# Kernel tuning notes

Measured on AMD Instinct MI355X. Metric: run time of the kernel, lower is better.

## Reference

```python
import jax, jax.numpy as jnp
import numpy as np
from jax import lax

B_SZ, SEQ, D_MODEL = 8, 2048, 1024
N_LAYER = 2
D_INNER = 2 * D_MODEL          # expand=2
D_STATE = 16
D_CONV = 4
DT_RANK = D_MODEL // 16        # ceil(1024/16)=64
EPS = 1e-5


def setup_inputs() -> dict:
    key = jax.random.key(0)
    ks = jax.random.split(key, 8)
    f = lambda k, shp, sc: jax.random.normal(k, shp, jnp.float32) * sc
    A_log = jnp.tile(jnp.log(jnp.arange(1, D_STATE + 1, dtype=jnp.float32)),
                     (N_LAYER, D_INNER, 1))  # S4D-real init, [L, d_inner, d_state]
    return {
        "x": f(ks[0], (B_SZ, SEQ, D_MODEL), 1.0),
        "in_proj_w": f(ks[1], (N_LAYER, 2 * D_INNER, D_MODEL), 0.02),
        "conv_w": f(ks[2], (N_LAYER, D_INNER, D_CONV), 0.2),
        "conv_b": jnp.zeros((N_LAYER, D_INNER), jnp.float32),
        "x_proj_w": f(ks[3], (N_LAYER, DT_RANK + 2 * D_STATE, D_INNER), 0.02),
        "dt_proj_w": f(ks[4], (N_LAYER, D_INNER, DT_RANK), 0.1),
        "dt_proj_b": f(ks[5], (N_LAYER, D_INNER), 0.5) - 4.0,  # softplus -> small dt
        "A_log": A_log,
        "D_param": jnp.ones((N_LAYER, D_INNER), jnp.float32),
        "out_proj_w": f(ks[6], (N_LAYER, D_MODEL, D_INNER), 0.02),
        "norm_w": jnp.ones((N_LAYER, D_MODEL), jnp.float32),
        "norm_b": jnp.zeros((N_LAYER, D_MODEL), jnp.float32),
    }


def _layer_norm(x, w, b):
    mu = jnp.mean(x, axis=-1, keepdims=True)
    var = jnp.mean(jnp.square(x - mu), axis=-1, keepdims=True)
    return (x - mu) * lax.rsqrt(var + EPS) * w + b


def _causal_dw_conv(x, w, b):
    # x: [B, Lq, d_inner], w: [d_inner, d_conv] depthwise causal conv
    xp = jnp.pad(x, ((0, 0), (D_CONV - 1, 0), (0, 0)))
    L = x.shape[1]
    y = b
    for k in range(D_CONV):
        y = y + xp[:, k:k + L, :] * w[:, k]
    return y


def _selective_scan(u, dt, Bm, Cm, A, Dp):
    # u, dt: [B, Lq, d_inner]; Bm, Cm: [B, Lq, d_state]; A: [d_inner, d_state]
    def step(h, inp):
        ut, dtt, Bt, Ct = inp                         # [B,di],[B,di],[B,ds],[B,ds]
        dA = jnp.exp(dtt[..., None] * A)              # [B, di, ds]
        h = dA * h + (dtt * ut)[..., None] * Bt[:, None, :]
        y = jnp.einsum('bds,bs->bd', h, Ct)
        return h, y

    h0 = jnp.zeros((u.shape[0], D_INNER, D_STATE), u.dtype)
    xs = (u.transpose(1, 0, 2), dt.transpose(1, 0, 2),
          Bm.transpose(1, 0, 2), Cm.transpose(1, 0, 2))
    _, ys = lax.scan(step, h0, xs)                    # ys: [Lq, B, di]
    return ys.transpose(1, 0, 2) + u * Dp


def _mamba(x, in_w, cw, cb, xpw, dtw, dtb, A_log, Dp, ow):
    xz = jnp.einsum('bld,ed->ble', x, in_w)           # [B, L, 2*d_inner]
    xi, z = jnp.split(xz, 2, axis=-1)
    xc = jax.nn.silu(_causal_dw_conv(xi, cw, cb))     # [B, L, d_inner]
    xdbl = jnp.einsum('bld,ed->ble', xc, xpw)         # [B, L, dt_rank+2*d_state]
    dt_low = xdbl[..., :DT_RANK]
    Bm = xdbl[..., DT_RANK:DT_RANK + D_STATE]
    Cm = xdbl[..., DT_RANK + D_STATE:]
    dt = jax.nn.softplus(jnp.einsum('blr,dr->bld', dt_low, dtw) + dtb)
    A = -jnp.exp(A_log)                               # [d_inner, d_state]
    y = _selective_scan(xc, dt, Bm, Cm, A, Dp)
    y = y * jax.nn.silu(z)
    return jnp.einsum('ble,de->bld', y, ow)           # [B, L, d_model]


def reference(x, in_proj_w, conv_w, conv_b, x_proj_w, dt_proj_w, dt_proj_b,
              A_log, D_param, out_proj_w, norm_w, norm_b):
    residual = None
    for l in range(N_LAYER):
        residual = x if residual is None else x + residual
        h = _layer_norm(residual, norm_w[l], norm_b[l])
        x = _mamba(h, in_proj_w[l], conv_w[l], conv_b[l], x_proj_w[l],
                   dt_proj_w[l], dt_proj_b[l], A_log[l], D_param[l], out_proj_w[l])
    # NOTE: source forward returns x without applying norm_f
    return x
```

## Files before the change

### kernel.cpp

```cpp
#include <hip/hip_runtime.h>
#include <cstddef>
#include <cstdint>

#define SEQB   8
#define SEQL   2048
#define DMODEL 1024
#define DINNER 2048
#define DSTATE 16
#define NC     32
#define TC     64
#define TT     8

typedef __attribute__((ext_vector_type(4))) float f32x4;
typedef __attribute__((ext_vector_type(8))) short bf16x8;
typedef unsigned int u32;
typedef const __attribute__((address_space(1))) u32* gas_ptr;
typedef __attribute__((address_space(3))) u32* las_ptr;

__device__ __forceinline__ void gld16(const void* g, void* l){
  __builtin_amdgcn_global_load_lds((gas_ptr)g, (las_ptr)l, 16, 0, 0);
}

__device__ __forceinline__ float siluf(float x){ return x / (1.f + __expf(-x)); }
__device__ __forceinline__ float softplusf(float x){ return (x > 20.f) ? x : log1pf(__expf(x)); }

__device__ __forceinline__ unsigned short f2bf_rne(float f){
  unsigned int u = __float_as_uint(f);
  u += 0x7FFFu + ((u>>16)&1u);
  return (unsigned short)(u>>16);
}
__device__ __forceinline__ void split_bf(float f, unsigned short& h, unsigned short& l){
  unsigned short hs = f2bf_rne(f);
  float hf = __uint_as_float(((unsigned int)hs)<<16);
  h = hs;
  l = f2bf_rne(f - hf);
}

__global__ __launch_bounds__(256)
void wsplit2(const float* __restrict__ src, unsigned short* __restrict__ dst,
             int K, int k4shift)
{
  int idx = blockIdx.x*256 + threadIdx.x;
  int r  = idx >> k4shift;
  int c4 = idx & ((1<<k4shift)-1);
  float4 v = ((const float4*)src)[idx];
  unsigned short h,l; short4 h4, l4;
  split_bf(v.x,h,l); h4.x=(short)h; l4.x=(short)l;
  split_bf(v.y,h,l); h4.y=(short)h; l4.y=(short)l;
  split_bf(v.z,h,l); h4.z=(short)h; l4.z=(short)l;
  split_bf(v.w,h,l); h4.w=(short)h; l4.w=(short)l;
  size_t ro = (size_t)r*2*K;
  *(short4*)&dst[ro + (c4<<2)]     = h4;
  *(short4*)&dst[ro + K + (c4<<2)] = l4;
}

__global__ __launch_bounds__(256)
void wsplit_og(const float* __restrict__ src, unsigned short* __restrict__ dst)
{
  int idx = blockIdx.x*256 + threadIdx.x;
  int r  = idx >> 9;
  int c4 = idx & 511;
  int layer = r >> 10, rr = r & 1023;
  float4 v = ((const float4*)src)[idx];
  unsigned short h,l; short4 h4, l4;
  split_bf(v.x,h,l); h4.x=(short)h; l4.x=(short)l;
  split_bf(v.y,h,l); h4.y=(short)h; l4.y=(short)l;
  split_bf(v.z,h,l); h4.z=(short)h; l4.z=(short)l;
  split_bf(v.w,h,l); h4.w=(short)h; l4.w=(short)l;
  int col = c4 << 2;
  int g = col >> 8, j = col & 255;
  size_t base = (size_t)layer*1024*4096 + (size_t)rr*4096 + g*512 + j;
  *(short4*)&dst[base]       = h4;
  *(short4*)&dst[base + 256] = l4;
}

__global__ __launch_bounds__(256)
void ln_split2(const float* __restrict__ a, const float* __restrict__ res,
               const float* __restrict__ w, const float* __restrict__ bias,
               unsigned short* __restrict__ Hs)
{
  int row = blockIdx.x;
  size_t off = (size_t)row * DMODEL;
  float4 v = ((const float4*)(a + off))[threadIdx.x];
  if (res){
    float4 u = ((const float4*)(res + off))[threadIdx.x];
    v.x += u.x; v.y += u.y; v.z += u.z; v.w += u.w;
  }
  float s  = v.x + v.y + v.z + v.w;
  float s2 = fmaf(v.x,v.x, fmaf(v.y,v.y, fmaf(v.z,v.z, v.w*v.w)));
  #pragma unroll
  for (int o=32;o>0;o>>=1){ s += __shfl_down(s,o,64); s2 += __shfl_down(s2,o,64); }
  __shared__ float red[8];
  int lane = threadIdx.x & 63, wid = threadIdx.x >> 6;
  if (lane==0){ red[wid]=s; red[4+wid]=s2; }
  __syncthreads();
  s  = red[0]+red[1]+red[2]+red[3];
  s2 = red[4]+red[5]+red[6]+red[7];
  float mu  = s * (1.f/DMODEL);
  float var = s2 * (1.f/DMODEL) - mu*mu;
  float rstd = rsqrtf(var + 1e-5f);
  float4 wv = ((const float4*)w)[threadIdx.x];
  float4 bv = ((const float4*)bias)[threadIdx.x];
  float4 o4;
  o4.x = (v.x-mu)*rstd*wv.x + bv.x;
  o4.y = (v.y-mu)*rstd*wv.y + bv.y;
  o4.z = (v.z-mu)*rstd*wv.z + bv.z;
  o4.w = (v.w-mu)*rstd*wv.w + bv.w;
  unsigned short h,l; short4 h4, l4;
  split_bf(o4.x,h,l); h4.x=(short)h; l4.x=(short)l;
  split_bf(o4.y,h,l); h4.y=(short)h; l4.y=(short)l;
  split_bf(o4.z,h,l); h4.z=(short)h; l4.z=(short)l;
  split_bf(o4.w,h,l); h4.w=(short)h; l4.w=(short)l;
  size_t ro = (size_t)row*2048;
  int c = threadIdx.x<<2;
  *(short4*)&Hs[ro + c]        = h4;
  *(short4*)&Hs[ro + 1024 + c] = l4;
}

__global__ __launch_bounds__(256)
void mgemm_in(const unsigned short* __restrict__ A,
              const unsigned short* __restrict__ B,
              float* __restrict__ XI, float* __restrict__ ZB)
{
  __shared__ __align__(16) unsigned short As[128*64];
  __shared__ __align__(16) unsigned short Bs[128*64];
  const int t = threadIdx.x;
  const int mbase = blockIdx.y << 7, nbase = blockIdx.x << 7;

  const int lane = t & 63, w = t >> 6;
  const int wr = w >> 1, wc = w & 1;
  const int l16 = lane & 15, kq = lane >> 4;

  const int sr8 = lane >> 3, sl8 = lane & 7;
  const unsigned short* pA[4]; const unsigned short* pB[4];
  unsigned short* dA[4]; unsigned short* dB[4];
  #pragma unroll
  for (int c=0;c<4;c++){
    int row = c*32 + w*8 + sr8;
    int ss  = sl8 ^ (row & 7);
    int colb = (ss < 4) ? (ss<<3) : (1024 + ((ss-4)<<3));
    pA[c] = A + (size_t)(mbase+row)*2048 + colb;
    pB[c] = B + (size_t)(nbase+row)*2048 + colb;
    dA[c] = &As[row*64 + sl8*8];
    dB[c] = &Bs[row*64 + sl8*8];
  }

  f32x4 acc[4][4];
  #pragma unroll
  for (int i=0;i<4;i++)
    #pragma unroll
    for (int j=0;j<4;j++) acc[i][j] = (f32x4){0.f,0.f,0.f,0.f};

  for (int k0=0; k0<1024; k0+=32){
    #pragma unroll
    for (int c=0;c<4;c++){
      gld16(pA[c] + k0, dA[c]);
      gld16(pB[c] + k0, dB[c]);
    }
    __syncthreads();
    bf16x8 ah[4], al[4];
    #pragma unroll
    for (int mf=0; mf<4; mf++){
      int ra = wr*64 + mf*16 + l16;
      ah[mf] = *(const bf16x8*)&As[ra*64 + (( kq      ^ (ra&7))<<3)];
      al[mf] = *(const bf16x8*)&As[ra*64 + (((kq+4)   ^ (ra&7))<<3)];
    }
    #pragma unroll
    for (int nf=0; nf<4; nf++){
      int rb = wc*64 + nf*16 + l16;
      bf16x8 bh = *(const bf16x8*)&Bs[rb*64 + (( kq    ^ (rb&7))<<3)];
      bf16x8 bl = *(const bf16x8*)&Bs[rb*64 + (((kq+4) ^ (rb&7))<<3)];
      #pragma unroll
      for (int mf=0; mf<4; mf++){
        acc[mf][nf] = __builtin_amdgcn_mfma_f32_16x16x32_bf16(ah[mf], bh, acc[mf][nf], 0,0,0);
        acc[mf][nf] = __builtin_amdgcn_mfma_f32_16x16x32_bf16(ah[mf], bl, acc[mf][nf], 0,0,0);
        acc[mf][nf] = __builtin_amdgcn_mfma_f32_16x16x32_bf16(al[mf], bh, acc[mf][nf], 0,0,0);
      }
    }
    __syncthreads();
  }

  float* Cd = (nbase < 2048) ? XI : ZB;
  const int cb = (nbase < 2048) ? nbase : (nbase - 2048);
  #pragma unroll
  for (int mf=0; mf<4; mf++){
    int r0 = mbase + wr*64 + mf*16 + kq*4;
    #pragma unroll
    for (int nf=0; nf<4; nf++){
      int c = cb + wc*64 + nf*16 + l16;
      #pragma unroll
      for (int r=0;r<4;r++)
        Cd[(size_t)(r0+r)*2048 + c] = acc[mf][nf][r];
    }
  }
}

__global__ __launch_bounds__(256)
void mgemm_out3(const unsigned short* __restrict__ A,
                const unsigned short* __restrict__ B,
                float* __restrict__ C)
{
  __shared__ __align__(16) unsigned short As[128*64];
  __shared__ __align__(16) unsigned short Bs[128*64];
  const int t = threadIdx.x;
  const int mbase = blockIdx.y << 7, nbase = blockIdx.x << 7;

  const int lane = t & 63, w = t >> 6;
  const int wr = w >> 1, wc = w & 1;
  const int l16 = lane & 15, kq = lane >> 4;

  const int sr8 = lane >> 3, sl8 = lane & 7;
  const unsigned short* pA[4]; const unsigned short* pB[4];
  unsigned short* dA[4]; unsigned short* dB[4];
  #pragma unroll
  for (int c=0;c<4;c++){
    int row = c*32 + w*8 + sr8;
    int ss  = sl8 ^ (row & 7);
    int pofs = (ss < 4) ? (ss<<3) : (256 + ((ss-4)<<3));
    pA[c] = A + (size_t)(mbase+row)*4096 + pofs;
    pB[c] = B + (size_t)(nbase+row)*4096 + pofs;
    dA[c] = &As[row*64 + sl8*8];
    dB[c] = &Bs[row*64 + sl8*8];
  }

  f32x4 acc[4][4];
  #pragma unroll
  for (int i=0;i<4;i++)
    #pragma unroll
    for (int j=0;j<4;j++) acc[i][j] = (f32x4){0.f,0.f,0.f,0.f};

  for (int k0=0; k0<2048; k0+=32){
    const int gso = ((k0>>8)<<9) + (k0 & 255);
    #pragma unroll
    for (int c=0;c<4;c++){
      gld16(pA[c] + gso, dA[c]);
      gld16(pB[c] + gso, dB[c]);
    }
    __syncthreads();
    bf16x8 ah[4], al[4];
    #pragma unroll
    for (int mf=0; mf<4; mf++){
      int ra = wr*64 + mf*16 + l16;
      ah[mf] = *(const bf16x8*)&As[ra*64 + (( kq      ^ (ra&7))<<3)];
      al[mf] = *(const bf16x8*)&As[ra*64 + (((kq+4)   ^ (ra&7))<<3)];
    }
    #pragma unroll
    for (int nf=0; nf<4; nf++){
      int rb = wc*64 + nf*16 + l16;
      bf16x8 bh = *(const bf16x8*)&Bs[rb*64 + (( kq    ^ (rb&7))<<3)];
      bf16x8 bl = *(const bf16x8*)&Bs[rb*64 + (((kq+4) ^ (rb&7))<<3)];
      #pragma unroll
      for (int mf=0; mf<4; mf++){
        acc[mf][nf] = __builtin_amdgcn_mfma_f32_16x16x32_bf16(ah[mf], bh, acc[mf][nf], 0,0,0);
        acc[mf][nf] = __builtin_amdgcn_mfma_f32_16x16x32_bf16(ah[mf], bl, acc[mf][nf], 0,0,0);
        acc[mf][nf] = __builtin_amdgcn_mfma_f32_16x16x32_bf16(al[mf], bh, acc[mf][nf], 0,0,0);
      }
    }
    __syncthreads();
  }

  #pragma unroll
  for (int mf=0; mf<4; mf++){
    int r0 = mbase + wr*64 + mf*16 + kq*4;
    #pragma unroll
    for (int nf=0; nf<4; nf++){
      int c = nbase + wc*64 + nf*16 + l16;
      #pragma unroll
      for (int r=0;r<4;r++)
        C[(size_t)(r0+r)*1024 + c] = acc[mf][nf][r];
    }
  }
}

__global__ __launch_bounds__(256)
void xproj_pair(const unsigned short* __restrict__ A,
                const unsigned short* __restrict__ W2,
                float* __restrict__ XD)
{
  __shared__ __align__(16) unsigned short S[128*64];
  const int t = threadIdx.x;
  const int mbase = blockIdx.x << 5;
  const int lane = t & 63, w = t >> 6;
  const int mf = w & 1, nc0 = (w >> 1) * 48;
  const int l16 = lane & 15, kq = lane >> 4;

  const unsigned short* ps[4]; unsigned short* ds[4];
  #pragma unroll
  for (int c=0;c<4;c++){
    int idx = c*256 + t;
    int row = idx >> 3, sl8 = idx & 7;
    int ss  = sl8 ^ (row & 7);
    int colb = (ss < 4) ? (ss<<3) : (2048 + ((ss-4)<<3));
    ps[c] = (row < 32) ? (A + (size_t)(mbase+row)*4096 + colb)
                       : (W2 + (size_t)(row-32)*4096 + colb);
    ds[c] = &S[row*64 + sl8*8];
  }

  f32x4 acc[3];
  #pragma unroll
  for (int j=0;j<3;j++) acc[j] = (f32x4){0.f,0.f,0.f,0.f};

  for (int k0=0; k0<2048; k0+=32){
    #pragma unroll
    for (int c=0;c<4;c++) gld16(ps[c] + k0, ds[c]);
    __syncthreads();
    int ra = mf*16 + l16;
    bf16x8 ah = *(const bf16x8*)&S[ra*64 + (( kq    ^ (ra&7))<<3)];
    bf16x8 al = *(const bf16x8*)&S[ra*64 + (((kq+4) ^ (ra&7))<<3)];
    #pragma unroll
    for (int nf=0; nf<3; nf++){
      int rb = 32 + nc0 + nf*16 + l16;
      bf16x8 bh = *(const bf16x8*)&S[rb*64 + (( kq    ^ (rb&7))<<3)];
      bf16x8 bl = *(const bf16x8*)&S[rb*64 + (((kq+4) ^ (rb&7))<<3)];
      acc[nf] = __builtin_amdgcn_mfma_f32_16x16x32_bf16(ah, bh, acc[nf], 0,0,0);
      acc[nf] = __builtin_amdgcn_mfma_f32_16x16x32_bf16(ah, bl, acc[nf], 0,0,0);
      acc[nf] = __builtin_amdgcn_mfma_f32_16x16x32_bf16(al, bh, acc[nf], 0,0,0);
    }
    __syncthreads();
  }
  #pragma unroll
  for (int nf=0; nf<3; nf++){
    int c = nc0 + nf*16 + l16;
    int r0s = mbase + mf*16 + kq*4;
    #pragma unroll
    for (int r=0;r<4;r++)
      XD[(size_t)(r0s+r)*96 + c] = acc[nf][r];
  }
}

__global__ __launch_bounds__(256)
void gemm_dt(const float* __restrict__ A, int lda,
             const float* __restrict__ B, int ldb,
             float* __restrict__ C, int ldc,
             int K, const float* __restrict__ ebias)
{
  __shared__ float As[16][132];
  __shared__ float Bs[16][132];
  int tid = threadIdx.x;
  int tx = tid & 15, ty = tid >> 4;
  int mbase = blockIdx.y << 7;
  int nbase = blockIdx.x << 7;
  float acc[8][8];
  #pragma unroll
  for (int i=0;i<8;i++)
    #pragma unroll
    for (int j=0;j<8;j++) acc[i][j]=0.f;

  for (int k0=0;k0<K;k0+=16){
    #pragma unroll
    for (int it=0; it<2; it++){
      int idx = tid + (it<<8);
      int row = idx >> 2;
      int kq  = (idx & 3) << 2;
      float4 va = *(const float4*)(A + (size_t)(mbase+row)*lda + k0 + kq);
      As[kq+0][row]=va.x; As[kq+1][row]=va.y; As[kq+2][row]=va.z; As[kq+3][row]=va.w;
      float4 vb = *(const float4*)(B + (size_t)(nbase+row)*ldb + k0 + kq);
      Bs[kq+0][row]=vb.x; Bs[kq+1][row]=vb.y; Bs[kq+2][row]=vb.z; Bs[kq+3][row]=vb.w;
    }
    __syncthreads();
    #pragma unroll
    for (int k=0;k<16;k++){
      float a[8], bb[8];
      *(float4*)&a[0]  = *(const float4*)&As[k][ty<<2];
      *(float4*)&a[4]  = *(const float4*)&As[k][64+(ty<<2)];
      *(float4*)&bb[0] = *(const float4*)&Bs[k][tx<<2];
      *(float4*)&bb[4] = *(const float4*)&Bs[k][64+(tx<<2)];
      #pragma unroll
      for (int i=0;i<8;i++)
        #pragma unroll
        for (int j=0;j<8;j++)
          acc[i][j] = fmaf(a[i], bb[j], acc[i][j]);
    }
    __syncthreads();
  }

  int n0 = nbase + (tx<<2);
  int n1 = n0 + 64;
  float4 eb0 = *(const float4*)(ebias + n0);
  float4 eb1 = *(const float4*)(ebias + n1);
  #pragma unroll
  for (int i=0;i<8;i++){
    int mrow = mbase + ((i<4) ? ((ty<<2)+i) : (64 + (ty<<2) + (i-4)));
    float4 c0 = make_float4(acc[i][0],acc[i][1],acc[i][2],acc[i][3]);
    float4 c1 = make_float4(acc[i][4],acc[i][5],acc[i][6],acc[i][7]);
    c0.x = softplusf(c0.x+eb0.x); c0.y = softplusf(c0.y+eb0.y);
    c0.z = softplusf(c0.z+eb0.z); c0.w = softplusf(c0.w+eb0.w);
    c1.x = softplusf(c1.x+eb1.x); c1.y = softplusf(c1.y+eb1.y);
    c1.z = softplusf(c1.z+eb1.z); c1.w = softplusf(c1.w+eb1.w);
    *(float4*)(C + (size_t)mrow*ldc + n0) = c0;
    *(float4*)(C + (size_t)mrow*ldc + n1) = c1;
  }
}

__global__ __launch_bounds__(256)
void conv_silu_kernel(const float* __restrict__ xi, const float* __restrict__ cw,
                      const float* __restrict__ cb, unsigned short* __restrict__ u2)
{
  const int row = blockIdx.x;
  const int d0 = threadIdx.x << 3;
  const int tt = row & (SEQL-1);

  float wk[4][8];
  {
    const float4* cw4 = (const float4*)(cw + (size_t)d0*4);
    #pragma unroll
    for (int j=0;j<8;j++){
      float4 wj = cw4[j];
      wk[0][j]=wj.x; wk[1][j]=wj.y; wk[2][j]=wj.z; wk[3][j]=wj.w;
    }
  }
  float bias[8];
  *(float4*)&bias[0] = *(const float4*)(cb + d0);
  *(float4*)&bias[4] = *(const float4*)(cb + d0 + 4);

  const float* base = xi + (size_t)row*DINNER + d0;
  float r0[8], r1[8], r2[8], r3[8];
#define LD8(dst, p) { *(float4*)&dst[0] = ((const float4*)(p))[0]; \
                      *(float4*)&dst[4] = ((const float4*)(p))[1]; }
  LD8(r0, base);
  if (tt>=1){ LD8(r1, base-DINNER); }   else { for(int j=0;j<8;j++) r1[j]=0.f; }
  if (tt>=2){ LD8(r2, base-2*DINNER); } else { for(int j=0;j<8;j++) r2[j]=0.f; }
  if (tt>=3){ LD8(r3, base-3*DINNER); } else { for(int j=0;j<8;j++) r3[j]=0.f; }
#undef LD8

  unsigned short h8[8], l8[8];
  #pragma unroll
  for (int j=0;j<8;j++){
    float y = fmaf(r0[j], wk[3][j], fmaf(r1[j], wk[2][j],
              fmaf(r2[j], wk[1][j], fmaf(r3[j], wk[0][j], bias[j]))));
    float uv = siluf(y);
    split_bf(uv, h8[j], l8[j]);
  }
  unsigned short* outp = u2 + (size_t)row*4096 + d0;
  *(uint4*)outp          = *(const uint4*)h8;
  *(uint4*)(outp + 2048) = *(const uint4*)l8;
}

template<int PASS>
__global__ __launch_bounds__(256)
void scan_chunk(const unsigned short* __restrict__ u2, float* __restrict__ dty,
                const float* __restrict__ xdbl, const float* __restrict__ zb,
                const float* __restrict__ A_log, const float* __restrict__ Dp,
                float* __restrict__ hfin, float* __restrict__ sumdt)
{
  __shared__ __align__(16) float Tdt[2][TT][256];
  __shared__ __align__(16) float Tu [2][TT][256];
  __shared__ __align__(16) float Tz [(PASS==3)?2:1][(PASS==3)?TT:1][(PASS==3)?256:4];
  __shared__ __align__(16) float Tbc[2][TT][32];

  const int tid = threadIdx.x;
  const int idx = blockIdx.x*256 + tid;
  const int d = idx & (DINNER-1);
  const int g = idx >> 11;
  const int cck = g & (NC-1);
  const int bb = g >> 5;
  const int wv = tid >> 6, ln = tid & 63;
  const int dbase = (blockIdx.x << 8) & (DINNER-1);

  float A2[16];
  {
    const float* al = A_log + (size_t)d*DSTATE;
    #pragma unroll
    for (int s=0;s<16;s++) A2[s] = -expf(al[s]) * 1.44269504f;
  }
  float h[16];
  if (PASS == 1){
    #pragma unroll
    for (int s=0;s<16;s++) h[s] = 0.f;
  } else {
    const float* hp = hfin + ((size_t)g*DINNER + d)*16;
    #pragma unroll
    for (int s=0;s<16;s+=4) *(float4*)&h[s] = *(const float4*)(hp + s);
  }
  const float Dv = (PASS==3) ? Dp[d] : 0.f;

  const size_t row0 = (size_t)bb*SEQL + (size_t)cck*TC;

#define STAGE(buf, T0) do { \
    _Pragma("unroll") \
    for (int q=0;q<2;q++){ \
      int r = q*4 + wv; \
      size_t rowi = row0 + (T0) + r; \
      gld16(dty + rowi*2048 + dbase + ln*4, &Tdt[buf][r][0]); \
      const unsigned short* us = u2 + rowi*4096 + \
          ((ln < 32) ? (dbase + ln*8) : (2048 + dbase + (ln-32)*8)); \
      gld16(us, &Tu[buf][r][0]); \
      if (PASS==3) gld16(zb + rowi*2048 + dbase + ln*4, &Tz[buf][r][0]); \
    } \
    if (wv == 3){ \
      gld16(xdbl + (row0 + (T0) + (ln>>3))*96 + 64 + (ln&7)*4, &Tbc[buf][0][0]); \
    } \
  } while(0)

  STAGE(0, 0);
  asm volatile("s_waitcnt vmcnt(0)" ::: "memory");
  __builtin_amdgcn_s_barrier();
  __builtin_amdgcn_sched_barrier(0);

  float sdt = 0.f;

  for (int t0 = 0; t0 < TC; t0 += TT){
    const int cur = (t0 >> 3) & 1, nxt = cur ^ 1;
    const bool hasNext = (t0 + TT < TC);
    if (hasNext) STAGE(nxt, t0 + TT);

    if (hasNext){
      if (PASS==3){
        if (wv==3) asm volatile("s_waitcnt vmcnt(7)" ::: "memory");
        else       asm volatile("s_waitcnt vmcnt(6)" ::: "memory");
      } else {
        if (wv==3) asm volatile("s_waitcnt vmcnt(5)" ::: "memory");
        else       asm volatile("s_waitcnt vmcnt(4)" ::: "memory");
      }
    } else {
      asm volatile("s_waitcnt vmcnt(0)" ::: "memory");
    }
    __builtin_amdgcn_s_barrier();
    __builtin_amdgcn_sched_barrier(0);

    #pragma unroll
    for (int tt=0; tt<TT; tt++){
      float dtc = Tdt[cur][tt][tid];
      const unsigned short* tur = (const unsigned short*)&Tu[cur][tt][0];
      float uc = __uint_as_float((u32)tur[tid] << 16)
               + __uint_as_float((u32)tur[256+tid] << 16);
      float Bv[16], Cv[16];
      #pragma unroll
      for (int q=0;q<4;q++) *(float4*)&Bv[q*4] = *(const float4*)&Tbc[cur][tt][q*4];
      if (PASS==3){
        #pragma unroll
        for (int q=0;q<4;q++) *(float4*)&Cv[q*4] = *(const float4*)&Tbc[cur][tt][16+q*4];
      }
      if (PASS==1) sdt += dtc;
      float du = dtc*uc;
      float y = 0.f;
      #pragma unroll
      for (int s=0;s<16;s++){
        float dA = exp2f(dtc*A2[s]);
        h[s] = fmaf(dA, h[s], du*Bv[s]);
        if (PASS==3) y = fmaf(h[s], Cv[s], y);
      }
      if (PASS==3){
        float zc = Tz[cur][tt][tid];
        y = fmaf(uc, Dv, y);
        float gv = y * siluf(zc);
        unsigned short gh, gl;
        split_bf(gv, gh, gl);
        Tdt[cur][tt][tid] = __uint_as_float((u32)gh | ((u32)gl << 16));
      }
    }

    if (PASS==3) asm volatile("s_waitcnt lgkmcnt(0)" ::: "memory");
    __builtin_amdgcn_s_barrier();
    __builtin_amdgcn_sched_barrier(0);

    if (PASS==3){
      #pragma unroll
      for (int q=0;q<2;q++){
        int r = q*4 + wv;
        size_t rowi = row0 + t0 + r;
        const u32* T = (const u32*)&Tdt[cur][r][0];
        int o0 = ln*4;
        u32 vals[4];
        if (ln < 32){
          #pragma unroll
          for (int k=0;k<4;k++){
            int i2 = (o0+k)*2;
            vals[k] = (T[i2] & 0xFFFFu) | (T[i2+1] << 16);
          }
        } else {
          #pragma unroll
          for (int k=0;k<4;k++){
            int i2 = (o0+k-128)*2;
            vals[k] = (T[i2] >> 16) | (T[i2+1] & 0xFFFF0000u);
          }
        }
        *(float4*)(dty + rowi*2048 + dbase + o0) = *(const float4*)vals;
      }
    }
  }
#undef STAGE

  if (PASS==1){
    float* hp = hfin + ((size_t)g*DINNER + d)*16;
    #pragma unroll
    for (int s=0;s<16;s+=4) *(float4*)(hp + s) = *(const float4*)&h[s];
    sumdt[(size_t)g*DINNER + d] = sdt;
  }
}

__global__ __launch_bounds__(256)
void scan_prop(const float* __restrict__ A_log, float* __restrict__ hfin,
               const float* __restrict__ sumdt)
{
  int idx = blockIdx.x*256 + threadIdx.x;
  int s = idx & 15;
  int d = (idx >> 4) & (DINNER-1);
  int b = idx >> 15;
  float A2 = -expf(A_log[(size_t)d*DSTATE + s]) * 1.44269504f;
  float H = 0.f;
  size_t hbase = ((size_t)b*NC*DINNER + d)*16 + s;
  size_t sbase = (size_t)b*NC*DINNER + d;
  for (int c=0;c<NC;c++){
    float P   = exp2f(A2 * sumdt[sbase + (size_t)c*DINNER]);
    float tmp = hfin[hbase + (size_t)c*DINNER*16];
    hfin[hbase + (size_t)c*DINNER*16] = H;
    H = fmaf(P, H, tmp);
  }
}

extern "C" void kernel_launch(void* const* d_in, const int* in_sizes, int n_in,
                              void* d_out, int out_size, void* d_ws, size_t ws_size,
                              hipStream_t stream)
{
  const float* x    = (const float*)d_in[0];
  const float* in_w = (const float*)d_in[1];
  const float* cw   = (const float*)d_in[2];
  const float* cb   = (const float*)d_in[3];
  const float* xpw  = (const float*)d_in[4];
  const float* dtw  = (const float*)d_in[5];
  const float* dtb  = (const float*)d_in[6];
  const float* A_log= (const float*)d_in[7];
  const float* Dp   = (const float*)d_in[8];
  const float* ow   = (const float*)d_in[9];
  const float* nw   = (const float*)d_in[10];
  const float* nb   = (const float*)d_in[11];
  float* outF = (float*)d_out;

  const size_t fixedB = 33554432ULL + 16777216ULL + 1572864ULL;
  const size_t perB   = 58720256ULL;
  int NB = 4;
  while (NB > 1 && fixedB + (size_t)NB*perB > ws_size) NB >>= 1;
  const int Mc = NB * SEQL;
  const int nchunk = SEQB / NB;

  unsigned short* INW2  = (unsigned short*)d_ws;
  unsigned short* OUTWG = INW2 + (size_t)2*4096*2048;
  unsigned short* XPW2  = OUTWG + (size_t)2*1024*4096;
  char* dyn = (char*)(XPW2 + (size_t)2*96*4096);

  unsigned short* SH = (unsigned short*)dyn;
  float* XD = (float*)dyn;
  float* HF = (float*)(dyn + (size_t)Mc*384);
  float* SD = (float*)(dyn + (size_t)Mc*2432);
  float* XI = (float*)(dyn + (size_t)Mc*4096);
  float* ZB = XI + (size_t)Mc*2048;
  unsigned short* U2 = (unsigned short*)(ZB + (size_t)Mc*2048);

  wsplit2<<<8192, 256, 0, stream>>>(in_w, INW2, 1024, 8);
  wsplit2<<<384,  256, 0, stream>>>(xpw,  XPW2, 2048, 9);
  wsplit_og<<<4096, 256, 0, stream>>>(ow, OUTWG);

  for (int c = 0; c < nchunk; ++c){
    const size_t rowoff = (size_t)c * Mc;
    const float* xrows = x + rowoff * DMODEL;
    float* X1 = outF + rowoff * DMODEL;

    for (int l = 0; l < 2; ++l){
      const float* Al = A_log + (size_t)l*DINNER*DSTATE;

      ln_split2<<<Mc, 256, 0, stream>>>(
          (l==0) ? xrows : X1, (l==0) ? nullptr : xrows,
          nw + (size_t)l*DMODEL, nb + (size_t)l*DMODEL, SH);

      mgemm_in<<<dim3(32, Mc/128), 256, 0, stream>>>(
          SH, INW2 + (size_t)l*4096*2048, XI, ZB);

      conv_silu_kernel<<<Mc, 256, 0, stream>>>(
          XI, cw + (size_t)l*DINNER*4, cb + (size_t)l*DINNER, U2);

      xproj_pair<<<Mc/32, 256, 0, stream>>>(
          U2, XPW2 + (size_t)l*96*4096, XD);

      gemm_dt<<<dim3(16, Mc/128), 256, 0, stream>>>(
          XD, 96, dtw + (size_t)l*DINNER*64, 64, XI, DINNER, 64,
          dtb + (size_t)l*DINNER);

      scan_chunk<1><<<NB*NC*8, 256, 0, stream>>>(
          U2, XI, XD, ZB, Al, Dp + (size_t)l*DINNER, HF, SD);
      scan_prop<<<NB*128, 256, 0, stream>>>(Al, HF, SD);
      scan_chunk<3><<<NB*NC*8, 256, 0, stream>>>(
          U2, XI, XD, ZB, Al, Dp + (size_t)l*DINNER, HF, SD);

      mgemm_out3<<<dim3(8, Mc/128), 256, 0, stream>>>(
          (const unsigned short*)XI, OUTWG + (size_t)l*1024*4096, X1);
    }
  }
}
```

Before: 3.307 ms.

## Move dt projection GEMM to split-bf16 MFMA and batch conv rows per block

Replaces the scalar fp32 FMA dt-projection GEMM with an MFMA kernel that splits both operands into high/low bf16 halves and accumulates three cross products to keep near-fp32 accuracy. The dt weights are pre-split once into a new workspace region, and activations are split on the fly while loading to LDS. Separately, the causal conv+SiLU kernel now processes four consecutive rows per block, so the overlapping history rows are loaded once instead of up to four times. The bf16x3 emulation carries a small accuracy risk, and the workspace budget grows slightly.

```diff
diff --git a/kernel.cpp b/kernel.cpp
--- a/kernel.cpp
+++ b/kernel.cpp
@@ -35,6 +35,20 @@
   h = hs;
   l = f2bf_rne(f - hf);
 }
+
+#define CV8P(PH, PSRC) { \
+  const float4* _p4 = (const float4*)(PSRC); \
+  float4 _a = _p4[0], _b = _p4[1]; \
+  bf16x8 _H, _L; unsigned short _h,_l; \
+  split_bf(_a.x,_h,_l); _H[0]=(short)_h; _L[0]=(short)_l; \
+  split_bf(_a.y,_h,_l); _H[1]=(short)_h; _L[1]=(short)_l; \
+  split_bf(_a.z,_h,_l); _H[2]=(short)_h; _L[2]=(short)_l; \
+  split_bf(_a.w,_h,_l); _H[3]=(short)_h; _L[3]=(short)_l; \
+  split_bf(_b.x,_h,_l); _H[4]=(short)_h; _L[4]=(short)_l; \
+  split_bf(_b.y,_h,_l); _H[5]=(short)_h; _L[5]=(short)_l; \
+  split_bf(_b.z,_h,_l); _H[6]=(short)_h; _L[6]=(short)_l; \
+  split_bf(_b.w,_h,_l); _H[7]=(short)_h; _L[7]=(short)_l; \
+  *(bf16x8*)(PH) = _H; *(bf16x8*)((unsigned short*)(PH) + 64) = _L; }
 
 __global__ __launch_bounds__(256)
 void wsplit2(const float* __restrict__ src, unsigned short* __restrict__ dst,
@@ -329,76 +343,94 @@
 }
 
 __global__ __launch_bounds__(256)
-void gemm_dt(const float* __restrict__ A, int lda,
-             const float* __restrict__ B, int ldb,
-             float* __restrict__ C, int ldc,
-             int K, const float* __restrict__ ebias)
-{
-  __shared__ float As[16][132];
-  __shared__ float Bs[16][132];
-  int tid = threadIdx.x;
-  int tx = tid & 15, ty = tid >> 4;
-  int mbase = blockIdx.y << 7;
-  int nbase = blockIdx.x << 7;
-  float acc[8][8];
-  #pragma unroll
-  for (int i=0;i<8;i++)
-    #pragma unroll
-    for (int j=0;j<8;j++) acc[i][j]=0.f;
-
-  for (int k0=0;k0<K;k0+=16){
-    #pragma unroll
-    for (int it=0; it<2; it++){
-      int idx = tid + (it<<8);
-      int row = idx >> 2;
-      int kq  = (idx & 3) << 2;
-      float4 va = *(const float4*)(A + (size_t)(mbase+row)*lda + k0 + kq);
-      As[kq+0][row]=va.x; As[kq+1][row]=va.y; As[kq+2][row]=va.z; As[kq+3][row]=va.w;
-      float4 vb = *(const float4*)(B + (size_t)(nbase+row)*ldb + k0 + kq);
-      Bs[kq+0][row]=vb.x; Bs[kq+1][row]=vb.y; Bs[kq+2][row]=vb.z; Bs[kq+3][row]=vb.w;
-    }
-    __syncthreads();
-    #pragma unroll
-    for (int k=0;k<16;k++){
-      float a[8], bb[8];
-      *(float4*)&a[0]  = *(const float4*)&As[k][ty<<2];
-      *(float4*)&a[4]  = *(const float4*)&As[k][64+(ty<<2)];
-      *(float4*)&bb[0] = *(const float4*)&Bs[k][tx<<2];
-      *(float4*)&bb[4] = *(const float4*)&Bs[k][64+(tx<<2)];
-      #pragma unroll
-      for (int i=0;i<8;i++)
+void mgemm_dt2(const float* __restrict__ XDf,
+               const unsigned short* __restrict__ DTW2,
+               float* __restrict__ XI,
+               const float* __restrict__ dtb)
+{
+  __shared__ __align__(16) unsigned short As[128*128];
+  __shared__ __align__(16) unsigned short Bs[128*128];
+  const int t = threadIdx.x;
+  const int mbase = blockIdx.y << 7, nbase = blockIdx.x << 7;
+  const int lane = t & 63, w = t >> 6;
+  const int wr = w >> 1, wc = w & 1;
+  const int l16 = lane & 15, kq = lane >> 4;
+
+  {
+    const int row = t >> 1, half = (t & 1) << 5;
+    const int r7 = row & 7;
+    const float* src = XDf + (size_t)(mbase + row)*96 + half;
+    #pragma unroll
+    for (int i=0;i<4;i++){
+      int g = (half >> 3) + i;
+      CV8P(&As[row*128 + ((g ^ r7)<<3)], src + i*8);
+    }
+  }
+  {
+    #pragma unroll
+    for (int q=0;q<8;q++){
+      int idx = q*256 + t;
+      int row = idx >> 4, sl = idx & 15;
+      int ss  = (sl & 8) | ((sl & 7) ^ (row & 7));
+      int col = (ss < 8) ? (ss<<3) : (64 + ((ss-8)<<3));
+      gld16(DTW2 + (size_t)(nbase+row)*128 + col, &Bs[row*128 + sl*8]);
+    }
+  }
+  __syncthreads();
+
+  f32x4 acc[4][4];
+  #pragma unroll
+  for (int i=0;i<4;i++)
+    #pragma unroll
+    for (int j=0;j<4;j++) acc[i][j] = (f32x4){0.f,0.f,0.f,0.f};
+
+  #pragma unroll
+  for (int kb=0; kb<3; kb++){
+    const int aoff = (kb==2) ? 8 : 0;
+    const int boff = (kb==1) ? 8 : 0;
+    #pragma unroll
+    for (int kw=0; kw<2; kw++){
+      const int sbase = kw*4 + kq;
+      bf16x8 af[4];
+      #pragma unroll
+      for (int mf=0; mf<4; mf++){
+        int ra = wr*64 + mf*16 + l16;
+        int sA = ((sbase ^ (ra&7)) + aoff);
+        af[mf] = *(const bf16x8*)&As[ra*128 + (sA<<3)];
+      }
+      #pragma unroll
+      for (int nf=0; nf<4; nf++){
+        int rb = wc*64 + nf*16 + l16;
+        int sB = ((sbase ^ (rb&7)) + boff);
+        bf16x8 bfr = *(const bf16x8*)&Bs[rb*128 + (sB<<3)];
         #pragma unroll
-        for (int j=0;j<8;j++)
-          acc[i][j] = fmaf(a[i], bb[j], acc[i][j]);
-    }
-    __syncthreads();
-  }
-
-  int n0 = nbase + (tx<<2);
-  int n1 = n0 + 64;
-  float4 eb0 = *(const float4*)(ebias + n0);
-  float4 eb1 = *(const float4*)(ebias + n1);
-  #pragma unroll
-  for (int i=0;i<8;i++){
-    int mrow = mbase + ((i<4) ? ((ty<<2)+i) : (64 + (ty<<2) + (i-4)));
-    float4 c0 = make_float4(acc[i][0],acc[i][1],acc[i][2],acc[i][3]);
-    float4 c1 = make_float4(acc[i][4],acc[i][5],acc[i][6],acc[i][7]);
-    c0.x = softplusf(c0.x+eb0.x); c0.y = softplusf(c0.y+eb0.y);
-    c0.z = softplusf(c0.z+eb0.z); c0.w = softplusf(c0.w+eb0.w);
-    c1.x = softplusf(c1.x+eb1.x); c1.y = softplusf(c1.y+eb1.y);
-    c1.z = softplusf(c1.z+eb1.z); c1.w = softplusf(c1.w+eb1.w);
-    *(float4*)(C + (size_t)mrow*ldc + n0) = c0;
-    *(float4*)(C + (size_t)mrow*ldc + n1) = c1;
-  }
-}
-
-__global__ __launch_bounds__(256)
-void conv_silu_kernel(const float* __restrict__ xi, const float* __restrict__ cw,
-                      const float* __restrict__ cb, unsigned short* __restrict__ u2)
-{
-  const int row = blockIdx.x;
+        for (int mf=0; mf<4; mf++)
+          acc[mf][nf] = __builtin_amdgcn_mfma_f32_16x16x32_bf16(af[mf], bfr, acc[mf][nf], 0,0,0);
+      }
+    }
+  }
+
+  #pragma unroll
+  for (int mf=0; mf<4; mf++){
+    int r0 = mbase + wr*64 + mf*16 + kq*4;
+    #pragma unroll
+    for (int nf=0; nf<4; nf++){
+      int c = nbase + wc*64 + nf*16 + l16;
+      float eb = dtb[c];
+      #pragma unroll
+      for (int r=0;r<4;r++)
+        XI[(size_t)(r0+r)*2048 + c] = softplusf(acc[mf][nf][r] + eb);
+    }
+  }
+}
+
+__global__ __launch_bounds__(256)
+void conv_silu4(const float* __restrict__ xi, const float* __restrict__ cw,
+                const float* __restrict__ cb, unsigned short* __restrict__ u2)
+{
+  const int r0 = blockIdx.x << 2;
   const int d0 = threadIdx.x << 3;
-  const int tt = row & (SEQL-1);
+  const int tt0 = r0 & (SEQL-1);
 
   float wk[4][8];
   {
@@ -413,27 +445,35 @@
   *(float4*)&bias[0] = *(const float4*)(cb + d0);
   *(float4*)&bias[4] = *(const float4*)(cb + d0 + 4);
 
-  const float* base = xi + (size_t)row*DINNER + d0;
-  float r0[8], r1[8], r2[8], r3[8];
+  float v[7][8];
 #define LD8(dst, p) { *(float4*)&dst[0] = ((const float4*)(p))[0]; \
                       *(float4*)&dst[4] = ((const float4*)(p))[1]; }
-  LD8(r0, base);
-  if (tt>=1){ LD8(r1, base-DINNER); }   else { for(int j=0;j<8;j++) r1[j]=0.f; }
-  if (tt>=2){ LD8(r2, base-2*DINNER); } else { for(int j=0;j<8;j++) r2[j]=0.f; }
-  if (tt>=3){ LD8(r3, base-3*DINNER); } else { for(int j=0;j<8;j++) r3[j]=0.f; }
+  #pragma unroll
+  for (int k=0;k<7;k++){
+    int trel = tt0 - 3 + k;
+    if (trel >= 0){
+      LD8(v[k], xi + (size_t)(r0 - 3 + k)*DINNER + d0);
+    } else {
+      #pragma unroll
+      for (int j=0;j<8;j++) v[k][j] = 0.f;
+    }
+  }
 #undef LD8
 
-  unsigned short h8[8], l8[8];
-  #pragma unroll
-  for (int j=0;j<8;j++){
-    float y = fmaf(r0[j], wk[3][j], fmaf(r1[j], wk[2][j],
-              fmaf(r2[j], wk[1][j], fmaf(r3[j], wk[0][j], bias[j]))));
-    float uv = siluf(y);
-    split_bf(uv, h8[j], l8[j]);
-  }
-  unsigned short* outp = u2 + (size_t)row*4096 + d0;
-  *(uint4*)outp          = *(const uint4*)h8;
-  *(uint4*)(outp + 2048) = *(const uint4*)l8;
+  #pragma unroll
+  for (int jrow=0; jrow<4; jrow++){
+    unsigned short h8[8], l8[8];
+    #pragma unroll
+    for (int j=0;j<8;j++){
+      float y = fmaf(v[jrow+3][j], wk[3][j], fmaf(v[jrow+2][j], wk[2][j],
+                fmaf(v[jrow+1][j], wk[1][j], fmaf(v[jrow][j], wk[0][j], bias[j]))));
+      float uv = siluf(y);
+      split_bf(uv, h8[j], l8[j]);
+    }
+    unsigned short* outp = u2 + (size_t)(r0 + jrow)*4096 + d0;
+    *(uint4*)outp          = *(const uint4*)h8;
+    *(uint4*)(outp + 2048) = *(const uint4*)l8;
+  }
 }
 
 template<int PASS>
@@ -627,7 +667,7 @@
   const float* nb   = (const float*)d_in[11];
   float* outF = (float*)d_out;
 
-  const size_t fixedB = 33554432ULL + 16777216ULL + 1572864ULL;
+  const size_t fixedB = 33554432ULL + 16777216ULL + 1572864ULL + 1048576ULL;
   const size_t perB   = 58720256ULL;
   int NB = 4;
   while (NB > 1 && fixedB + (size_t)NB*perB > ws_size) NB >>= 1;
@@ -637,7 +677,8 @@
   unsigned short* INW2  = (unsigned short*)d_ws;
   unsigned short* OUTWG = INW2 + (size_t)2*4096*2048;
   unsigned short* XPW2  = OUTWG + (size_t)2*1024*4096;
-  char* dyn = (char*)(XPW2 + (size_t)2*96*4096);
+  unsigned short* DTW2  = XPW2 + (size_t)2*96*4096;
+  char* dyn = (char*)(DTW2 + (size_t)2*2048*128);
 
   unsigned short* SH = (unsigned short*)dyn;
   float* XD = (float*)dyn;
@@ -649,6 +690,7 @@
 
   wsplit2<<<8192, 256, 0, stream>>>(in_w, INW2, 1024, 8);
   wsplit2<<<384,  256, 0, stream>>>(xpw,  XPW2, 2048, 9);
+  wsplit2<<<256,  256, 0, stream>>>(dtw,  DTW2, 64, 4);
   wsplit_og<<<4096, 256, 0, stream>>>(ow, OUTWG);
 
   for (int c = 0; c < nchunk; ++c){
@@ -666,15 +708,14 @@
       mgemm_in<<<dim3(32, Mc/128), 256, 0, stream>>>(
           SH, INW2 + (size_t)l*4096*2048, XI, ZB);
 
-      conv_silu_kernel<<<Mc, 256, 0, stream>>>(
+      conv_silu4<<<Mc/4, 256, 0, stream>>>(
           XI, cw + (size_t)l*DINNER*4, cb + (size_t)l*DINNER, U2);
 
       xproj_pair<<<Mc/32, 256, 0, stream>>>(
           U2, XPW2 + (size_t)l*96*4096, XD);
 
-      gemm_dt<<<dim3(16, Mc/128), 256, 0, stream>>>(
-          XD, 96, dtw + (size_t)l*DINNER*64, 64, XI, DINNER, 64,
-          dtb + (size_t)l*DINNER);
+      mgemm_dt2<<<dim3(16, Mc/128), 256, 0, stream>>>(
+          XD, DTW2 + (size_t)l*2048*128, XI, dtb + (size_t)l*DINNER);
 
       scan_chunk<1><<<NB*NC*8, 256, 0, stream>>>(
           U2, XI, XD, ZB, Al, Dp + (size_t)l*DINNER, HF, SD);
```

Result: faster. 3.159 ms (-4.5%).
